# Kernel tuning notes

Measured on AMD Instinct MI355X. Metric: run time of the kernel, lower is better.

Reference implementation:

```python
import jax, jax.numpy as jnp
import numpy as np

DIM = 512
HEADS = 8
DH = DIM // HEADS          # 64
M = DIM // 2               # 256 landmarks
PINV_ITERS = 6
KERNEL = 33                # residual_conv_kernel (lucidrains default)
SCALE = DH ** -0.5
LN_EPS = 1e-5


def setup_inputs() -> dict:
    key = jax.random.key(0)
    ks = jax.random.split(key, 6)
    b, n = 4, 4096
    x = jax.random.normal(ks[0], (b, n, DIM), jnp.float32)
    ln_w = jnp.ones((DIM,), jnp.float32)
    ln_b = jnp.zeros((DIM,), jnp.float32)
    w_qkv = jax.random.normal(ks[1], (DIM, 3 * DIM), jnp.float32) / np.float32(np.sqrt(DIM))
    w_out = jax.random.normal(ks[2], (DIM, DIM), jnp.float32) / np.float32(np.sqrt(DIM))
    b_out = jnp.zeros((DIM,), jnp.float32)
    # depthwise Conv2d(heads, heads, (33,1), groups=heads, bias=False): OIHW = (8,1,33,1)
    conv_w = jax.random.normal(ks[3], (HEADS, 1, KERNEL, 1), jnp.float32) / np.float32(np.sqrt(KERNEL))
    # admin_torch.as_module(8): residual x*omega + f(x), omega learnable scalar init sqrt(8)
    omega = jnp.asarray(np.sqrt(8.0), jnp.float32)
    return dict(x=x, ln_w=ln_w, ln_b=ln_b, w_qkv=w_qkv, w_out=w_out,
                b_out=b_out, conv_w=conv_w, omega=omega)


def _layernorm(x, w, b):
    mu = x.mean(-1, keepdims=True)
    var = x.var(-1, keepdims=True)
    return (x - mu) * jax.lax.rsqrt(var + LN_EPS) * w + b


def _moore_penrose_pinv(x, iters):
    # Newton-Schulz iteration, exactly as lucidrains nystrom-attention
    abs_x = jnp.abs(x)
    col = abs_x.sum(-1)
    row = abs_x.sum(-2)
    z = jnp.swapaxes(x, -1, -2) / (jnp.max(col) * jnp.max(row))
    I = jnp.eye(x.shape[-1], dtype=x.dtype)
    for _ in range(iters):
        xz = x @ z
        z = 0.25 * z @ (13. * I - xz @ (15. * I - xz @ (7. * I - xz)))
    return z


def reference(x, ln_w, ln_b, w_qkv, w_out, b_out, conv_w, omega):
    b, n, _ = x.shape
    nx = _layernorm(x, ln_w, ln_b)
    qkv = nx @ w_qkv                                # [b, n, 3*dim]
    q, k, v = jnp.split(qkv, 3, axis=-1)
    to_heads = lambda t: t.reshape(b, n, HEADS, DH).transpose(0, 2, 1, 3)  # bhnd
    q = to_heads(q) * SCALE
    k = to_heads(k)
    v = to_heads(v)
    l = n // M                                      # tokens per landmark group
    q_l = q.reshape(b, HEADS, M, l, DH).mean(3)     # [b,h,m,d]
    k_l = k.reshape(b, HEADS, M, l, DH).mean(3)
    sim1 = jnp.einsum('bhid,bhjd->bhij', q, k_l)    # [b,h,n,m]
    sim2 = jnp.einsum('bhid,bhjd->bhij', q_l, k_l)  # [b,h,m,m]
    sim3 = jnp.einsum('bhid,bhjd->bhij', q_l, k)    # [b,h,m,n]
    a1 = jax.nn.softmax(sim1, -1)
    a2 = jax.nn.softmax(sim2, -1)
    a3 = jax.nn.softmax(sim3, -1)
    a2_inv = _moore_penrose_pinv(a2, PINV_ITERS)
    out = (a1 @ a2_inv) @ (a3 @ v)                  # [b,h,n,d]
    # residual depthwise conv along the sequence dim of v
    res = jax.lax.conv_general_dilated(
        v, conv_w, window_strides=(1, 1),
        padding=((KERNEL // 2, KERNEL // 2), (0, 0)),
        dimension_numbers=('NCHW', 'OIHW', 'NCHW'),
        feature_group_count=HEADS)
    out = out + res
    out = out.transpose(0, 2, 1, 3).reshape(b, n, HEADS * DH)
    out = out @ w_out + b_out                       # to_out (dropout is eval no-op)
    return x * omega + out                          # admin residual
```

## Files before the change

kernel.cpp:

```cpp
#include <hip/hip_runtime.h>
#include <math.h>

#define B_    4
#define N_    4096
#define DIM_  512
#define H_    8
#define DH_   64
#define M_    256
#define LGRP  16
#define BH_   (B_*H_)
#define SCALE_ 0.125f
#define LN_EPS_ 1e-5f

#define SZ_QKVH (B_*H_*N_*DH_)
#define SZ_LM   (BH_*M_*DH_)
#define SZ_MM   (BH_*M_*M_)

typedef unsigned short ushort_t;
typedef __attribute__((ext_vector_type(8))) short bfrag8;
typedef __attribute__((ext_vector_type(4))) float fvec4;

__device__ __forceinline__ ushort_t f2b(float f) {
    unsigned u = __float_as_uint(f);
    unsigned r = (u + 0x7fffu + ((u >> 16) & 1u)) >> 16;
    return (ushort_t)r;
}
__device__ __forceinline__ float b2f(ushort_t s) {
    return __uint_as_float(((unsigned)s) << 16);
}

__device__ __forceinline__ void gload16(const ushort_t* g, ushort_t* l) {
    __builtin_amdgcn_global_load_lds(
        (const __attribute__((address_space(1))) void*)g,
        (__attribute__((address_space(3))) void*)l, 16, 0, 0);
}

__global__ __launch_bounds__(256) void ln_kernel(const float* __restrict__ x,
                                                 const float* __restrict__ w,
                                                 const float* __restrict__ bb,
                                                 ushort_t* __restrict__ nxb) {
    int row = blockIdx.x;
    int t = threadIdx.x;
    const float* xr = x + (size_t)row * DIM_;
    float v0 = xr[t], v1 = xr[t + 256];
    float s = v0 + v1, sq = v0 * v0 + v1 * v1;
    __shared__ float ls[4], lq[4];
    for (int off = 32; off > 0; off >>= 1) {
        s  += __shfl_down(s, off);
        sq += __shfl_down(sq, off);
    }
    int wid = t >> 6, lid = t & 63;
    if (lid == 0) { ls[wid] = s; lq[wid] = sq; }
    __syncthreads();
    if (t == 0) {
        float S = 0, Q = 0;
        for (int i = 0; i < 4; i++) { S += ls[i]; Q += lq[i]; }
        ls[0] = S; lq[0] = Q;
    }
    __syncthreads();
    float mean = ls[0] * (1.f / DIM_);
    float var  = lq[0] * (1.f / DIM_) - mean * mean;
    float rs = rsqrtf(var + LN_EPS_);
    ushort_t* o = nxb + (size_t)row * DIM_;
    o[t]       = f2b((v0 - mean) * rs * w[t]       + bb[t]);
    o[t + 256] = f2b((v1 - mean) * rs * w[t + 256] + bb[t + 256]);
}

__global__ __launch_bounds__(256) void tcast(const float* __restrict__ in,
                                             ushort_t* __restrict__ outT,
                                             int R, int C) {
    __shared__ float tile[32][33];
    int c0 = blockIdx.x * 32, r0 = blockIdx.y * 32;
    int t = threadIdx.x;
    #pragma unroll
    for (int u = 0; u < 4; u++) {
        int lin = t + 256 * u;
        int r = lin >> 5, c = lin & 31;
        tile[r][c] = in[(size_t)(r0 + r) * C + c0 + c];
    }
    __syncthreads();
    #pragma unroll
    for (int u = 0; u < 4; u++) {
        int lin = t + 256 * u;
        int cc = lin >> 5, rr = lin & 31;
        outT[(size_t)(c0 + cc) * R + r0 + rr] = f2b(tile[rr][cc]);
    }
}

template<int EPI>
__global__ __launch_bounds__(256) void gemm_bt128(const ushort_t* __restrict__ A,
                                                  const ushort_t* __restrict__ BT,
                                                  ushort_t* __restrict__ qb,
                                                  ushort_t* __restrict__ kb,
                                                  ushort_t* __restrict__ vb,
                                                  const float* __restrict__ x,
                                                  const float* __restrict__ bo,
                                                  const float* __restrict__ omega,
                                                  float* __restrict__ out) {
    const int K = 512;
    __shared__ __align__(16) ushort_t smem[4 * 128 * 64];
    int t = threadIdx.x;
    int lin = blockIdx.x + blockIdx.y * gridDim.x;
    int nwg = gridDim.x * gridDim.y;
    int wg  = (lin & 7) * (nwg >> 3) + (lin >> 3);
    int n0 = (wg % gridDim.x) * 128, m0 = (wg / gridDim.x) * 128;
    int w = t >> 6, lane = t & 63;
    int wr = (w >> 1) * 64, wc = (w & 1) * 64;
    int l15 = lane & 15, quad = lane >> 4, kq = quad * 8;
    int lrow = lane >> 3, lc8 = (lane & 7) * 8;
    int scol = lc8 ^ ((lrow & 7) << 3);
    int sw   = (l15 & 7) << 3;
    fvec4 acc[4][4] = {};

    auto stage = [&](int buf, int kc) {
        ushort_t* Ad = smem + buf * 16384;
        ushort_t* Bd = Ad + 8192;
        #pragma unroll
        for (int u = 0; u < 4; u++) {
            int r0 = (w << 5) + (u << 3);
            int row = r0 + lrow;
            const ushort_t* ga;
            if (EPI == 0) {
                ga = A + (size_t)(m0 + row) * K + kc + scol;
            } else {
                int grow = m0 + row; int b_ = grow >> 12, nn = grow & 4095;
                ga = A + (((size_t)(b_ * H_ + (kc >> 6)) * N_ + nn) << 6) + scol;
            }
            gload16(ga, Ad + r0 * 64);
            gload16(BT + (size_t)(n0 + row) * K + kc + scol, Bd + r0 * 64);
        }
    };

    stage(0, 0);
    __syncthreads();
    int cur = 0;
    for (int kt = 0; kt < 8; ++kt) {
        if (kt < 7) stage(cur ^ 1, (kt + 1) * 64);
        const ushort_t* As = smem + cur * 16384;
        const ushort_t* Bs = As + 8192;
        #pragma unroll
        for (int ks = 0; ks < 64; ks += 32) {
            int kcol = (ks + kq) ^ sw;
            bfrag8 a[4], b[4];
            #pragma unroll
            for (int r = 0; r < 4; r++) a[r] = *(bfrag8*)(As + (wr + r * 16 + l15) * 64 + kcol);
            #pragma unroll
            for (int c = 0; c < 4; c++) b[c] = *(bfrag8*)(Bs + (wc + c * 16 + l15) * 64 + kcol);
            #pragma unroll
            for (int r = 0; r < 4; r++)
                #pragma unroll
                for (int c = 0; c < 4; c++)
                    acc[r][c] = __builtin_amdgcn_mfma_f32_16x16x32_bf16(a[r], b[c], acc[r][c], 0, 0, 0);
        }
        __syncthreads();
        cur ^= 1;
    }

    if (EPI == 0) {
        int sec = n0 >> 9;
        float mul = (sec == 0) ? SCALE_ : 1.0f;
        ushort_t (*Ct)[132] = (ushort_t(*)[132])smem;
        #pragma unroll
        for (int r = 0; r < 4; r++) {
            #pragma unroll
            for (int reg = 0; reg < 4; reg++) {
                int lr = wr + r * 16 + quad * 4 + reg;
                #pragma unroll
                for (int c = 0; c < 4; c++) {
                    int lc = wc + c * 16 + l15;
                    Ct[lr][lc] = f2b(acc[r][c][reg] * mul);
                }
            }
        }
        __syncthreads();
        int row = t & 127, half = t >> 7;
        int grow = m0 + row; int b_ = grow >> 12, nn = grow & 4095;
        int head = ((n0 & 511) >> 6) + half;
        ushort_t* dstbuf = (sec == 0) ? qb : ((sec == 1) ? kb : vb);
        ushort_t* dp = dstbuf + (((size_t)(b_ * H_ + head) * N_ + nn) << 6);
        #pragma unroll
        for (int i = 0; i < 8; i++)
            *(uint4*)(dp + i * 8) = *(uint4*)&Ct[row][half * 64 + i * 8];
    } else {
        float om = omega[0];
        #pragma unroll
        for (int r = 0; r < 4; r++) {
            #pragma unroll
            for (int reg = 0; reg < 4; reg++) {
                int grow = m0 + wr + r * 16 + quad * 4 + reg;
                #pragma unroll
                for (int c = 0; c < 4; c++) {
                    int gcol = n0 + wc + c * 16 + l15;
                    size_t o = (size_t)grow * DIM_ + gcol;
                    out[o] = om * x[o] + bo[gcol] + acc[r][c][reg];
                }
            }
        }
    }
}

__global__ __launch_bounds__(256) void landmark_kernel(const ushort_t* __restrict__ q,
                                                       const ushort_t* __restrict__ k,
                                                       ushort_t* __restrict__ ql,
                                                       ushort_t* __restrict__ kl) {
    int idx = blockIdx.x * 256 + threadIdx.x;
    const ushort_t* src = blockIdx.y ? k : q;
    ushort_t* dst = blockIdx.y ? kl : ql;
    int d8 = (idx & 7) * 8;
    int m = (idx >> 3) & 255;
    int bh = idx >> 11;
    const ushort_t* p = src + (((size_t)bh * N_) + m * LGRP) * DH_ + d8;
    float s[8] = {};
    #pragma unroll
    for (int j = 0; j < LGRP; j++) {
        union { uint4 u4; ushort_t sv[8]; } val;
        val.u4 = *(const uint4*)(p + (size_t)j * DH_);
        #pragma unroll
        for (int e = 0; e < 8; e++) s[e] += b2f(val.sv[e]);
    }
    union { uint4 u4; ushort_t sv[8]; } o;
    #pragma unroll
    for (int e = 0; e < 8; e++) o.sv[e] = f2b(s[e] * (1.f / LGRP));
    *(uint4*)(dst + ((size_t)bh * M_ + m) * DH_ + d8) = o.u4;
}

__global__ __launch_bounds__(256) void sim2_softmax(const ushort_t* __restrict__ ql,
                                                    const ushort_t* __restrict__ kl,
                                                    float* __restrict__ a2,
                                                    ushort_t* __restrict__ a2b) {
    int i = blockIdx.x, bh = blockIdx.y, j = threadIdx.x;
    __shared__ float qrow[64];
    __shared__ float red[256];
    if (j < 64) qrow[j] = b2f(ql[((size_t)bh * M_ + i) * DH_ + j]);
    __syncthreads();
    const ushort_t* kr = kl + ((size_t)bh * M_ + j) * DH_;
    float s = 0;
    #pragma unroll
    for (int d = 0; d < 64; d++) s += qrow[d] * b2f(kr[d]);
    red[j] = s; __syncthreads();
    for (int off = 128; off > 0; off >>= 1) {
        if (j < off) red[j] = fmaxf(red[j], red[j + off]);
        __syncthreads();
    }
    float mx = red[0]; __syncthreads();
    float p = __expf(s - mx);
    red[j] = p; __syncthreads();
    for (int off = 128; off > 0; off >>= 1) {
        if (j < off) red[j] += red[j + off];
        __syncthreads();
    }
    float res = p / red[0];
    size_t o = ((size_t)bh * M_ + i) * M_ + j;
    a2[o] = res;
    a2b[o] = f2b(res);
}

__global__ __launch_bounds__(256) void colpart(const float* __restrict__ a2,
                                               float* __restrict__ cs2,
                                               unsigned* __restrict__ red) {
    int bh = blockIdx.x, s = blockIdx.y, t = threadIdx.x;
    if (bh == 0 && s == 0 && t == 0) red[0] = 0u;
    const float* A = a2 + ((size_t)bh << 16) + (size_t)s * 32 * M_;
    float cs = 0.f;
    #pragma unroll
    for (int i = 0; i < 32; i++) cs += A[(size_t)i * M_ + t];
    cs2[((size_t)s * BH_ + bh) * M_ + t] = cs;
}

__global__ __launch_bounds__(256) void colmax(const float* __restrict__ cs2, unsigned* red) {
    int bh = blockIdx.x, t = threadIdx.x;
    float v = 0.f;
    #pragma unroll
    for (int s = 0; s < 8; s++) v += cs2[((size_t)s * BH_ + bh) * M_ + t];
    __shared__ float lr[256];
    lr[t] = v; __syncthreads();
    for (int off = 128; off > 0; off >>= 1) {
        if (t < off) lr[t] = fmaxf(lr[t], lr[t + off]);
        __syncthreads();
    }
    if (t == 0) atomicMax(red, __float_as_uint(lr[0]));
}

__global__ __launch_bounds__(256) void pinv_init2(const float* __restrict__ a2,
                                                  const unsigned* __restrict__ red,
                                                  ushort_t* __restrict__ zA,
                                                  ushort_t* __restrict__ zAT) {
    __shared__ float tile[32][33];
    int bt = blockIdx.z; int j0 = blockIdx.x * 32, i0 = blockIdx.y * 32;
    float invd = 1.f / __uint_as_float(red[0]);
    const float* Ab = a2 + ((size_t)bt << 16);
    size_t bo = (size_t)bt << 16;
    int t = threadIdx.x;
    #pragma unroll
    for (int u = 0; u < 4; u++) {
        int lin = t + 256 * u; int r = lin >> 5, c = lin & 31;
        float vv = Ab[(size_t)(i0 + r) * M_ + j0 + c] * invd;
        tile[r][c] = vv;
        zAT[bo + (size_t)(i0 + r) * M_ + j0 + c] = f2b(vv);
    }
    __syncthreads();
    #pragma unroll
    for (int u = 0; u < 4; u++) {
        int lin = t + 256 * u; int cc = lin >> 5, rr = lin & 31;
        zA[bo + (size_t)(j0 + cc) * M_ + i0 + rr] = f2b(tile[rr][cc]);
    }
}

__global__ __launch_bounds__(256) void gemm_pinv(const ushort_t* __restrict__ A,
                                                 const ushort_t* __restrict__ BT,
                                                 ushort_t* __restrict__ outN,
                                                 ushort_t* __restrict__ outT,
                                                 ushort_t* __restrict__ outT1,
                                                 float* __restrict__ outF,
                                                 float coefI, float scale) {
    __shared__ __align__(16) ushort_t smem[2 * 16384];
    int t = threadIdx.x;
    int lin = blockIdx.x + (blockIdx.y << 2) + (blockIdx.z << 4);
    int wg  = (lin & 7) * 64 + (lin >> 3);
    int n0 = (wg & 3) * 64, m0 = ((wg >> 2) & 3) * 64;
    int bt = wg >> 4;
    const ushort_t* Ab = A + ((size_t)bt << 16);
    const ushort_t* Bb = BT + ((size_t)bt << 16);
    int w = t >> 6, lane = t & 63;
    int wr = (w >> 1) * 32, wc = (w & 1) * 32;
    int l15 = lane & 15, quad = lane >> 4, kq = quad * 8;
    int lrow = lane >> 3, lc8 = (lane & 7) * 8;
    int scol = lc8 ^ ((lrow & 7) << 3);
    int sw   = (l15 & 7) << 3;
    fvec4 acc[2][2] = {};

    #pragma unroll
    for (int c = 0; c < 4; c++) {
        #pragma unroll
        for (int u = 0; u < 2; u++) {
            int r0 = (w << 4) + (u << 3);
            int row = r0 + lrow;
            gload16(Ab + (size_t)(m0 + row) * M_ + c * 64 + scol, smem + c * 4096 + r0 * 64);
            gload16(Bb + (size_t)(n0 + row) * M_ + c * 64 + scol, smem + 16384 + c * 4096 + r0 * 64);
        }
    }
    __syncthreads();

    #pragma unroll
    for (int ks = 0; ks < 256; ks += 32) {
        const ushort_t* As = smem + (ks >> 6) * 4096;
        const ushort_t* Bs = As + 16384;
        int kcol = ((ks & 63) + kq) ^ sw;
        bfrag8 a[2], b[2];
        #pragma unroll
        for (int r = 0; r < 2; r++) a[r] = *(bfrag8*)(As + (wr + r * 16 + l15) * 64 + kcol);
        #pragma unroll
        for (int c = 0; c < 2; c++) b[c] = *(bfrag8*)(Bs + (wc + c * 16 + l15) * 64 + kcol);
        #pragma unroll
        for (int r = 0; r < 2; r++)
            #pragma unroll
            for (int c = 0; c < 2; c++)
                acc[r][c] = __builtin_amdgcn_mfma_f32_16x16x32_bf16(a[r], b[c], acc[r][c], 0, 0, 0);
    }
    __syncthreads();

    size_t bto = (size_t)bt << 16;
    if (outN || outF) {
        #pragma unroll
        for (int r = 0; r < 2; r++) {
            #pragma unroll
            for (int reg = 0; reg < 4; reg++) {
                int grow = m0 + wr + r * 16 + quad * 4 + reg;
                #pragma unroll
                for (int c = 0; c < 2; c++) {
                    int gcol = n0 + wc + c * 16 + l15;
                    float cv = scale * acc[r][c][reg] + (grow == gcol ? coefI : 0.f);
                    if (outN) outN[bto + (size_t)grow * M_ + gcol] = f2b(cv);
                    if (outF) outF[bto + (size_t)grow * M_ + gcol] = cv;
                }
            }
        }
    }
    if (outT || outT1) {
        ushort_t (*Ct)[65] = (ushort_t(*)[65])&smem[0];
        #pragma unroll
        for (int r = 0; r < 2; r++) {
            #pragma unroll
            for (int reg = 0; reg < 4; reg++) {
                int lr = wr + r * 16 + quad * 4 + reg;
                #pragma unroll
                for (int c = 0; c < 2; c++) {
                    int lc = wc + c * 16 + l15;
                    float cv = scale * acc[r][c][reg] + ((m0 + lr) == (n0 + lc) ? coefI : 0.f);
                    Ct[lr][lc] = f2b(cv);
                }
            }
        }
        __syncthreads();
        int j = t & 63, quarter = t >> 6, i0 = quarter * 16;
        #pragma unroll
        for (int vq = 0; vq < 2; vq++) {
            union { uint4 u4; ushort_t s[8]; } o1, o2;
            #pragma unroll
            for (int e = 0; e < 8; e++) {
                int il = i0 + vq * 8 + e;
                ushort_t bv = Ct[il][j];
                o1.s[e] = bv;
                o2.s[e] = f2b(((m0 + il) == (n0 + j) ? 7.f : 0.f) - b2f(bv));
            }
            size_t dst = bto + (size_t)(n0 + j) * M_ + m0 + i0 + vq * 8;
            if (outT)  *(uint4*)&outT[dst]  = o1.u4;
            if (outT1) *(uint4*)&outT1[dst] = o2.u4;
        }
    }
}

__global__ __launch_bounds__(256) void flash_a3v(const ushort_t* __restrict__ Q,
                                                 const ushort_t* __restrict__ K,
                                                 const ushort_t* __restrict__ V,
                                                 float* __restrict__ Opart,
                                                 float* __restrict__ lout) {
    const int nk = N_;
    const int CHUNK = N_ / 8;
    int bh = blockIdx.y, ch = blockIdx.x;
    int j0 = ch * CHUNK, j1 = j0 + CHUNK;

    __shared__ __align__(16) ushort_t smem[4 * 64 * 72];
    ushort_t (*ks)[72]  = (ushort_t(*)[72])smem;
    ushort_t (*vts)[72] = (ushort_t(*)[72])(smem + 64 * 72);
    ushort_t (*pb)[64][72] = (ushort_t(*)[64][72])(smem + 2 * 64 * 72);

    int t = threadIdx.x;
    int w = t >> 6, lane = t & 63;
    int l15 = lane & 15, quad = lane >> 4, kq = quad * 8;
    int wrow = w * 16;

    bfrag8 aq[4][2];
    const ushort_t* Qb = Q + (size_t)bh * M_ * DH_;
    #pragma unroll
    for (int s = 0; s < 4; s++) {
        #pragma unroll
        for (int u = 0; u < 2; u++) {
            int lin = t + 256 * u;
            int r = lin >> 3, cc = (lin & 7) * 8;
            *(uint4*)&pb[0][r][cc] = *(const uint4*)(Qb + (size_t)(s * 64 + r) * DH_ + cc);
        }
        __syncthreads();
        aq[s][0] = *(bfrag8*)&pb[0][wrow + l15][kq];
        aq[s][1] = *(bfrag8*)&pb[0][wrow + l15][32 + kq];
        __syncthreads();
    }

    fvec4 Oacc[4][4];
    #pragma unroll
    for (int s = 0; s < 4; s++)
        #pragma unroll
        for (int nt = 0; nt < 4; nt++)
            #pragma unroll
            for (int reg = 0; reg < 4; reg++) Oacc[s][nt][reg] = 0.f;
    float l_[4][4];
    #pragma unroll
    for (int s = 0; s < 4; s++)
        #pragma unroll
        for (int reg = 0; reg < 4; reg++) l_[s][reg] = 0.f;

    uint4 kreg[2], vreg[2];
    auto loadkv = [&](int j) {
        const ushort_t* Kb = K + ((size_t)bh * nk + j) * DH_;
        const ushort_t* Vb = V + ((size_t)bh * nk + j) * DH_;
        #pragma unroll
        for (int u = 0; u < 2; u++) {
            int lin = t + 256 * u;
            int r = lin >> 3, cc = (lin & 7) * 8;
            kreg[u] = *(const uint4*)(Kb + (size_t)r * DH_ + cc);
            vreg[u] = *(const uint4*)(Vb + (size_t)r * DH_ + cc);
        }
    };

    loadkv(j0);
    for (int j = j0; j < j1; j += 64) {
        #pragma unroll
        for (int u = 0; u < 2; u++) {
            int lin = t + 256 * u;
            int r = lin >> 3, cc = (lin & 7) * 8;
            *(uint4*)&ks[r][cc] = kreg[u];
            union { uint4 u4; ushort_t s[8]; } vv;
            vv.u4 = vreg[u];
            #pragma unroll
            for (int m = 0; m < 8; m++) vts[cc + m][r] = vv.s[m];
        }
        __syncthreads();
        if (j + 64 < j1) loadkv(j + 64);

        bfrag8 kb0[4], kb1[4], vb0[4], vb1[4];
        #pragma unroll
        for (int ct = 0; ct < 4; ct++) {
            kb0[ct] = *(bfrag8*)&ks[ct * 16 + l15][kq];
            kb1[ct] = *(bfrag8*)&ks[ct * 16 + l15][32 + kq];
            vb0[ct] = *(bfrag8*)&vts[ct * 16 + l15][kq];
            vb1[ct] = *(bfrag8*)&vts[ct * 16 + l15][32 + kq];
        }

        #pragma unroll
        for (int s = 0; s < 4; s++) {
            fvec4 S[4];
            #pragma unroll
            for (int ct = 0; ct < 4; ct++)
                #pragma unroll
                for (int reg = 0; reg < 4; reg++) S[ct][reg] = 0.f;
            #pragma unroll
            for (int ct = 0; ct < 4; ct++) {
                S[ct] = __builtin_amdgcn_mfma_f32_16x16x32_bf16(aq[s][0], kb0[ct], S[ct], 0, 0, 0);
                S[ct] = __builtin_amdgcn_mfma_f32_16x16x32_bf16(aq[s][1], kb1[ct], S[ct], 0, 0, 0);
            }
            float ps[4] = {0.f, 0.f, 0.f, 0.f};
            #pragma unroll
            for (int ct = 0; ct < 4; ct++) {
                #pragma unroll
                for (int reg = 0; reg < 4; reg++) {
                    float pv = __expf(S[ct][reg]);
                    ps[reg] += pv;
                    pb[s & 1][wrow + quad * 4 + reg][ct * 16 + l15] = f2b(pv);
                }
            }
            #pragma unroll
            for (int reg = 0; reg < 4; reg++) {
                float sm = ps[reg];
                sm += __shfl_xor(sm, 1);
                sm += __shfl_xor(sm, 2);
                sm += __shfl_xor(sm, 4);
                sm += __shfl_xor(sm, 8);
                l_[s][reg] += sm;
            }
            bfrag8 ap0 = *(bfrag8*)&pb[s & 1][wrow + l15][kq];
            bfrag8 ap1 = *(bfrag8*)&pb[s & 1][wrow + l15][32 + kq];
            #pragma unroll
            for (int nt = 0; nt < 4; nt++) {
                Oacc[s][nt] = __builtin_amdgcn_mfma_f32_16x16x32_bf16(ap0, vb0[nt], Oacc[s][nt], 0, 0, 0);
                Oacc[s][nt] = __builtin_amdgcn_mfma_f32_16x16x32_bf16(ap1, vb1[nt], Oacc[s][nt], 0, 0, 0);
            }
        }
        __syncthreads();
    }

    float (*Of)[68] = (float(*)[68])smem;
    const size_t R = (size_t)BH_ * M_;
    size_t rowbase = (size_t)ch * R + (size_t)bh * M_;
    #pragma unroll
    for (int s = 0; s < 4; s++) {
        __syncthreads();
        #pragma unroll
        for (int reg = 0; reg < 4; reg++) {
            #pragma unroll
            for (int nt = 0; nt < 4; nt++)
                Of[wrow + quad * 4 + reg][nt * 16 + l15] = Oacc[s][nt][reg];
        }
        if (l15 == 0) {
            #pragma unroll
            for (int reg = 0; reg < 4; reg++)
                lout[rowbase + s * 64 + wrow + quad * 4 + reg] = l_[s][reg];
        }
        __syncthreads();
        int orow = t >> 2, oc = (t & 3) * 16;
        float* Od = Opart + (rowbase + s * 64 + orow) * DH_ + oc;
        #pragma unroll
        for (int i = 0; i < 4; i++) {
            float4 v4 = make_float4(Of[orow][oc + i * 4], Of[orow][oc + i * 4 + 1],
                                    Of[orow][oc + i * 4 + 2], Of[orow][oc + i * 4 + 3]);
            *(float4*)(Od + i * 4) = v4;
        }
    }
}

__global__ __launch_bounds__(256) void flash_combine(const float* __restrict__ apart,
                                                     const float* __restrict__ lpart,
                                                     ushort_t* __restrict__ a3vb) {
    int idx = blockIdx.x * 256 + threadIdx.x;
    int d = idx & 63; int row = idx >> 6;
    const int R = BH_ * M_;
    size_t e = (size_t)row * DH_ + d;
    const size_t CH = (size_t)R * DH_;
    float l = 0.f, o = 0.f;
    #pragma unroll
    for (int s = 0; s < 8; s++) {
        l += lpart[row + (size_t)s * R];
        o += apart[e + (size_t)s * CH];
    }
    a3vb[e] = f2b(o / l);
}

__global__ __launch_bounds__(256) void flash_big(const ushort_t* __restrict__ Q,
                                                 const ushort_t* __restrict__ K,
                                                 const ushort_t* __restrict__ VT,
                                                 ushort_t* __restrict__ Obf) {
    const int nq = N_, nk = M_;
    int bh = blockIdx.y;
    int q0 = blockIdx.x * 256;
    __shared__ __align__(16) ushort_t ks[64][72];
    __shared__ __align__(16) ushort_t vts[64][72];
    __shared__ __align__(16) ushort_t pb[2][64][72];

    int t = threadIdx.x;
    int w = t >> 6, lane = t & 63;
    int l15 = lane & 15, quad = lane >> 4, kq = quad * 8;
    int wrow = w * 16;

    bfrag8 aq[4][2];
    const ushort_t* Qb = Q + ((size_t)bh * nq + q0) * DH_;
    #pragma unroll
    for (int s = 0; s < 4; s++) {
        #pragma unroll
        for (int u = 0; u < 2; u++) {
            int lin = t + 256 * u;
            int r = lin >> 3, cc = (lin & 7) * 8;
            *(uint4*)&pb[0][r][cc] = *(const uint4*)(Qb + (size_t)(s * 64 + r) * DH_ + cc);
        }
        __syncthreads();
        aq[s][0] = *(bfrag8*)&pb[0][wrow + l15][kq];
        aq[s][1] = *(bfrag8*)&pb[0][wrow + l15][32 + kq];
        __syncthreads();
    }

    fvec4 Oacc[4][4];
    #pragma unroll
    for (int s = 0; s < 4; s++)
        #pragma unroll
        for (int nt = 0; nt < 4; nt++)
            #pragma unroll
            for (int reg = 0; reg < 4; reg++) Oacc[s][nt][reg] = 0.f;
    float l_[4][4];
    #pragma unroll
    for (int s = 0; s < 4; s++)
        #pragma unroll
        for (int reg = 0; reg < 4; reg++) l_[s][reg] = 0.f;

    const ushort_t* VTb = VT + (size_t)bh * DH_ * nk;
    uint4 kreg[2], vreg[2];
    auto loadkv = [&](int j) {
        const ushort_t* Kb = K + ((size_t)bh * nk + j) * DH_;
        #pragma unroll
        for (int u = 0; u < 2; u++) {
            int lin = t + 256 * u;
            int r = lin >> 3, cc = (lin & 7) * 8;
            kreg[u] = *(const uint4*)(Kb + (size_t)r * DH_ + cc);
            vreg[u] = *(const uint4*)(VTb + (size_t)r * nk + j + cc);
        }
    };

    loadkv(0);
    for (int j = 0; j < nk; j += 64) {
        #pragma unroll
        for (int u = 0; u < 2; u++) {
            int lin = t + 256 * u;
            int r = lin >> 3, cc = (lin & 7) * 8;
            *(uint4*)&ks[r][cc] = kreg[u];
            *(uint4*)&vts[r][cc] = vreg[u];
        }
        __syncthreads();
        if (j + 64 < nk) loadkv(j + 64);

        bfrag8 kb0[4], kb1[4], vb0[4], vb1[4];
        #pragma unroll
        for (int ct = 0; ct < 4; ct++) {
            kb0[ct] = *(bfrag8*)&ks[ct * 16 + l15][kq];
            kb1[ct] = *(bfrag8*)&ks[ct * 16 + l15][32 + kq];
            vb0[ct] = *(bfrag8*)&vts[ct * 16 + l15][kq];
            vb1[ct] = *(bfrag8*)&vts[ct * 16 + l15][32 + kq];
        }

        #pragma unroll
        for (int s = 0; s < 4; s++) {
            fvec4 S[4];
            #pragma unroll
            for (int ct = 0; ct < 4; ct++)
                #pragma unroll
                for (int reg = 0; reg < 4; reg++) S[ct][reg] = 0.f;
            #pragma unroll
            for (int ct = 0; ct < 4; ct++) {
                S[ct] = __builtin_amdgcn_mfma_f32_16x16x32_bf16(aq[s][0], kb0[ct], S[ct], 0, 0, 0);
                S[ct] = __builtin_amdgcn_mfma_f32_16x16x32_bf16(aq[s][1], kb1[ct], S[ct], 0, 0, 0);
            }
            float ps[4] = {0.f, 0.f, 0.f, 0.f};
            #pragma unroll
            for (int ct = 0; ct < 4; ct++) {
                #pragma unroll
                for (int reg = 0; reg < 4; reg++) {
                    float pv = __expf(S[ct][reg]);
                    ps[reg] += pv;
                    pb[s & 1][wrow + quad * 4 + reg][ct * 16 + l15] = f2b(pv);
                }
            }
            #pragma unroll
            for (int reg = 0; reg < 4; reg++) {
                float sm = ps[reg];
                sm += __shfl_xor(sm, 1);
                sm += __shfl_xor(sm, 2);
                sm += __shfl_xor(sm, 4);
                sm += __shfl_xor(sm, 8);
                l_[s][reg] += sm;
            }
            bfrag8 ap0 = *(bfrag8*)&pb[s & 1][wrow + l15][kq];
            bfrag8 ap1 = *(bfrag8*)&pb[s & 1][wrow + l15][32 + kq];
            #pragma unroll
            for (int nt = 0; nt < 4; nt++) {
                Oacc[s][nt] = __builtin_amdgcn_mfma_f32_16x16x32_bf16(ap0, vb0[nt], Oacc[s][nt], 0, 0, 0);
                Oacc[s][nt] = __builtin_amdgcn_mfma_f32_16x16x32_bf16(ap1, vb1[nt], Oacc[s][nt], 0, 0, 0);
            }
        }
        __syncthreads();
    }

    ushort_t* Ob = Obf + ((size_t)bh * nq + q0) * DH_;
    #pragma unroll
    for (int s = 0; s < 4; s++) {
        #pragma unroll
        for (int reg = 0; reg < 4; reg++) {
            float inv = 1.f / l_[s][reg];
            #pragma unroll
            for (int nt = 0; nt < 4; nt++)
                pb[0][wrow + quad * 4 + reg][nt * 16 + l15] = f2b(Oacc[s][nt][reg] * inv);
        }
        __syncthreads();
        #pragma unroll
        for (int u = 0; u < 2; u++) {
            int lin = t + 256 * u;
            int r = lin >> 3, i = (lin & 7) * 8;
            *(uint4*)(Ob + (size_t)(s * 64 + r) * DH_ + i) = *(uint4*)&pb[0][r][i];
        }
        __syncthreads();
    }
}

__global__ __launch_bounds__(256) void wm_mfma(const ushort_t* __restrict__ Z,
                                               const ushort_t* __restrict__ A3V,
                                               ushort_t* __restrict__ WmT) {
    __shared__ __align__(16) ushort_t As[64][72];
    __shared__ __align__(16) ushort_t Bs[64][72];
    int bh = blockIdx.y;
    int i0 = blockIdx.x * 64;
    const ushort_t* Zb = Z + ((size_t)bh << 16);
    const ushort_t* Ab = A3V + ((size_t)bh << 14);
    int t = threadIdx.x;
    int w = t >> 6, lane = t & 63;
    int wr = (w >> 1) * 32, wc = (w & 1) * 32;
    int l15 = lane & 15, quad = lane >> 4, kq = quad * 8;
    fvec4 acc[2][2] = {};
    int rbase = t >> 3, c8 = (t & 7) * 8;

    for (int kc = 0; kc < M_; kc += 64) {
        #pragma unroll
        for (int u = 0; u < 2; u++) {
            int rr = rbase + 32 * u;
            *(float4*)&Bs[rr][c8] = *(const float4*)(Zb + (size_t)(i0 + rr) * M_ + kc + c8);
            union { uint4 u4; ushort_t s[8]; } av;
            av.u4 = *(const uint4*)(Ab + (size_t)(kc + rr) * DH_ + c8);
            #pragma unroll
            for (int m = 0; m < 8; m++) As[c8 + m][rr] = av.s[m];
        }
        __syncthreads();
        #pragma unroll
        for (int ks = 0; ks < 64; ks += 32) {
            bfrag8 a[2], b[2];
            #pragma unroll
            for (int r = 0; r < 2; r++) a[r] = *(bfrag8*)&As[wr + r * 16 + l15][ks + kq];
            #pragma unroll
            for (int c = 0; c < 2; c++) b[c] = *(bfrag8*)&Bs[wc + c * 16 + l15][ks + kq];
            #pragma unroll
            for (int r = 0; r < 2; r++)
                #pragma unroll
                for (int c = 0; c < 2; c++)
                    acc[r][c] = __builtin_amdgcn_mfma_f32_16x16x32_bf16(a[r], b[c], acc[r][c], 0, 0, 0);
        }
        __syncthreads();
    }
    #pragma unroll
    for (int r = 0; r < 2; r++) {
        #pragma unroll
        for (int reg = 0; reg < 4; reg++) {
            int drow = wr + r * 16 + quad * 4 + reg;
            ushort_t* dp = WmT + ((size_t)bh * DH_ + drow) * M_;
            #pragma unroll
            for (int c = 0; c < 2; c++)
                dp[i0 + wc + c * 16 + l15] = f2b(acc[r][c][reg]);
        }
    }
}

__global__ __launch_bounds__(256) void conv_kernel(const ushort_t* __restrict__ V,
                                                   const float* __restrict__ cw,
                                                   const ushort_t* __restrict__ ctxb,
                                                   ushort_t* __restrict__ outb) {
    int bh = blockIdx.y;
    int h = bh & 7;
    int i0 = blockIdx.x * 64;
    __shared__ float vb[96][64];
    __shared__ float wloc[33];
    int t = threadIdx.x;
    if (t < 33) wloc[t] = cw[h * 33 + t];
    #pragma unroll
    for (int u = 0; u < 3; u++) {
        int lin = t + 256 * u;
        int r = lin >> 3, cc = (lin & 7) * 8;
        int gi = i0 - 16 + r;
        union { uint4 u4; ushort_t s[8]; } val;
        if (gi >= 0 && gi < N_)
            val.u4 = *(const uint4*)(V + ((size_t)bh * N_ + gi) * DH_ + cc);
        else
            val.u4 = make_uint4(0, 0, 0, 0);
        #pragma unroll
        for (int m = 0; m < 8; m++) vb[r][cc + m] = b2f(val.s[m]);
    }
    __syncthreads();
    int d = t & 63, rb = t >> 6;
    for (int u = 0; u < 16; u++) {
        int r = rb * 16 + u;
        float s = 0.f;
        #pragma unroll
        for (int kk = 0; kk < 33; kk++) s += wloc[kk] * vb[r + kk][d];
        size_t o = ((size_t)bh * N_ + i0 + r) * DH_ + d;
        outb[o] = f2b(b2f(ctxb[o]) + s);
    }
}

extern "C" void kernel_launch(void* const* d_in, const int* in_sizes, int n_in,
                              void* d_out, int out_size, void* d_ws, size_t ws_size,
                              hipStream_t stream) {
    const float* x      = (const float*)d_in[0];
    const float* ln_w   = (const float*)d_in[1];
    const float* ln_b   = (const float*)d_in[2];
    const float* w_qkv  = (const float*)d_in[3];
    const float* w_out  = (const float*)d_in[4];
    const float* b_out  = (const float*)d_in[5];
    const float* conv_w = (const float*)d_in[6];
    const float* omega  = (const float*)d_in[7];
    float* out = (float*)d_out;

    float* fp = (float*)d_ws;
    float* a2    = fp;              fp += SZ_MM;
    float* apart = fp;              fp += SZ_QKVH / 2;
    float* lpart = fp;              fp += 8 * BH_ * M_;
    float* cs2   = fp;              fp += 8 * BH_ * M_;
    ushort_t* us = (ushort_t*)fp;
    ushort_t* wqkvT = us;           us += DIM_ * 3 * DIM_;
    ushort_t* woT   = us;           us += DIM_ * DIM_;
    ushort_t* a2b   = us;           us += SZ_MM;
    ushort_t* zA    = us;           us += SZ_MM;
    ushort_t* zAT   = us;           us += SZ_MM;
    ushort_t* zB    = us;           us += SZ_MM;
    ushort_t* zBT   = us;           us += SZ_MM;
    ushort_t* qb    = us;           us += SZ_QKVH;
    ushort_t* kb    = us;           us += SZ_QKVH;
    ushort_t* vb    = us;           us += SZ_QKVH;
    ushort_t* ctxb  = us;           us += SZ_QKVH;
    ushort_t* outhb = us;           us += SZ_QKVH;
    ushort_t* ql    = us;           us += SZ_LM;
    ushort_t* kl    = us;           us += SZ_LM;
    ushort_t* WmT   = us;           us += SZ_LM;
    ushort_t* a3vb  = us;           us += SZ_LM;
    unsigned* red   = (unsigned*)us;
    ushort_t* nxb = outhb;
    ushort_t* xz  = ctxb;
    ushort_t* t1T = xz  + SZ_MM;
    ushort_t* t2T = t1T + SZ_MM;
    ushort_t* t3T = t2T + SZ_MM;

    ln_kernel<<<B_ * N_, 256, 0, stream>>>(x, ln_w, ln_b, nxb);
    tcast<<<dim3(48, 16), 256, 0, stream>>>(w_qkv, wqkvT, DIM_, 3 * DIM_);
    tcast<<<dim3(16, 16), 256, 0, stream>>>(w_out, woT, DIM_, DIM_);
    gemm_bt128<0><<<dim3(12, 128), 256, 0, stream>>>(nxb, wqkvT, qb, kb, vb,
                                                     nullptr, nullptr, nullptr, nullptr);
    landmark_kernel<<<dim3(256, 2), 256, 0, stream>>>(qb, kb, ql, kl);
    sim2_softmax<<<dim3(M_, BH_), 256, 0, stream>>>(ql, kl, a2, a2b);
    colpart<<<dim3(BH_, 8), 256, 0, stream>>>(a2, cs2, red);
    colmax<<<BH_, 256, 0, stream>>>(cs2, red);
    pinv_init2<<<dim3(8, 8, 32), 256, 0, stream>>>(a2, red, zA, zAT);

    ushort_t* za = zA;  ushort_t* zaT = zAT;
    ushort_t* zb = zB;  ushort_t* zbT = zBT;
    for (int it = 0; it < 6; it++) {
        gemm_pinv<<<dim3(4, 4, BH_), 256, 0, stream>>>(a2b, zaT, xz, nullptr, t1T, nullptr, 0.f, 1.f);
        gemm_pinv<<<dim3(4, 4, BH_), 256, 0, stream>>>(xz, t1T, nullptr, t2T, nullptr, nullptr, 15.f, -1.f);
        gemm_pinv<<<dim3(4, 4, BH_), 256, 0, stream>>>(xz, t2T, nullptr, t3T, nullptr, nullptr, 13.f, -1.f);
        gemm_pinv<<<dim3(4, 4, BH_), 256, 0, stream>>>(za, t3T, zb, (it < 5) ? zbT : nullptr,
                                                       nullptr, nullptr, 0.f, 0.25f);
        ushort_t* tp;
        tp = za; za = zb; zb = tp;
        tp = zaT; zaT = zbT; zbT = tp;
    }

    flash_a3v<<<dim3(8, BH_), 256, 0, stream>>>(ql, kb, vb, apart, lpart);
    flash_combine<<<(BH_ * M_ * DH_) / 256, 256, 0, stream>>>(apart, lpart, a3vb);
    wm_mfma<<<dim3(4, BH_), 256, 0, stream>>>(za, a3vb, WmT);
    flash_big<<<dim3(N_ / 256, BH_), 256, 0, stream>>>(qb, kl, WmT, ctxb);
    conv_kernel<<<dim3(N_ / 64, BH_), 256, 0, stream>>>(vb, conv_w, ctxb, outhb);
    gemm_bt128<1><<<dim3(4, 128), 256, 0, stream>>>(outhb, woT, nullptr, nullptr, nullptr,
                                                    x, b_out, omega, out);
}
```

Baseline: 471.7 us.

## Fuse depthwise residual conv into flash_big epilogue and drop conv kernel

The 33-tap depthwise convolution over V is now computed in flash_big's output epilogue. Each block stages a 96-row bf16 V window in shared memory, writes the normalized attention output as fp32 to shared memory, and adds the conv sum before storing bf16 once. This removes the separate conv kernel launch and the bf16 round-trip of the intermediate context tensor through global memory. It also drops one bf16 rounding of the context before the add. The risk is that the V staging buffer is aliased onto ks but is larger than ks, so it relies on the following shared arrays lying contiguously. The epilogue also runs a serial 33-tap loop per 64-row slice inside the attention kernel.

```diff
diff --git a/kernel.cpp b/kernel.cpp
--- a/kernel.cpp
+++ b/kernel.cpp
@@ -587,6 +587,8 @@
 __global__ __launch_bounds__(256) void flash_big(const ushort_t* __restrict__ Q,
                                                  const ushort_t* __restrict__ K,
                                                  const ushort_t* __restrict__ VT,
+                                                 const ushort_t* __restrict__ V,
+                                                 const float* __restrict__ cw,
                                                  ushort_t* __restrict__ Obf) {
     const int nq = N_, nk = M_;
     int bh = blockIdx.y;
@@ -594,11 +596,13 @@
     __shared__ __align__(16) ushort_t ks[64][72];
     __shared__ __align__(16) ushort_t vts[64][72];
     __shared__ __align__(16) ushort_t pb[2][64][72];
+    __shared__ float wloc[33];
 
     int t = threadIdx.x;
     int w = t >> 6, lane = t & 63;
     int l15 = lane & 15, quad = lane >> 4, kq = quad * 8;
     int wrow = w * 16;
+    if (t < 33) wloc[t] = cw[(bh & 7) * 33 + t];
 
     bfrag8 aq[4][2];
     const ushort_t* Qb = Q + ((size_t)bh * nq + q0) * DH_;
@@ -705,24 +709,42 @@
         __syncthreads();
     }
 
+    ushort_t (*vstg)[64] = (ushort_t(*)[64])&ks[0][0];
+    float (*Of)[68] = (float(*)[68])&pb[0][0][0];
     ushort_t* Ob = Obf + ((size_t)bh * nq + q0) * DH_;
+    const ushort_t* Vb = V + (size_t)bh * nq * DH_;
+    int d = t & 63, rb = t >> 6;
     #pragma unroll
     for (int s = 0; s < 4; s++) {
+        __syncthreads();
+        #pragma unroll
+        for (int u = 0; u < 3; u++) {
+            int lin = t + 256 * u;
+            int r = lin >> 3, cc = (lin & 7) * 8;
+            int gi = q0 + 64 * s - 16 + r;
+            union { uint4 u4; ushort_t sv[8]; } val;
+            if (gi >= 0 && gi < N_)
+                val.u4 = *(const uint4*)(Vb + (size_t)gi * DH_ + cc);
+            else
+                val.u4 = make_uint4(0, 0, 0, 0);
+            *(uint4*)&vstg[r][cc] = val.u4;
+        }
         #pragma unroll
         for (int reg = 0; reg < 4; reg++) {
             float inv = 1.f / l_[s][reg];
             #pragma unroll
             for (int nt = 0; nt < 4; nt++)
-                pb[0][wrow + quad * 4 + reg][nt * 16 + l15] = f2b(Oacc[s][nt][reg] * inv);
-        }
-        __syncthreads();
-        #pragma unroll
-        for (int u = 0; u < 2; u++) {
-            int lin = t + 256 * u;
-            int r = lin >> 3, i = (lin & 7) * 8;
-            *(uint4*)(Ob + (size_t)(s * 64 + r) * DH_ + i) = *(uint4*)&pb[0][r][i];
-        }
-        __syncthreads();
+                Of[wrow + quad * 4 + reg][nt * 16 + l15] = Oacc[s][nt][reg] * inv;
+        }
+        __syncthreads();
+        #pragma unroll
+        for (int u = 0; u < 16; u++) {
+            int r = rb * 16 + u;
+            float cs = 0.f;
+            #pragma unroll
+            for (int kk = 0; kk < 33; kk++) cs += wloc[kk] * b2f(vstg[r + kk][d]);
+            Ob[(size_t)(s * 64 + r) * DH_ + d] = f2b(Of[r][d] + cs);
+        }
     }
 }
 
@@ -778,42 +800,6 @@
             for (int c = 0; c < 2; c++)
                 dp[i0 + wc + c * 16 + l15] = f2b(acc[r][c][reg]);
         }
-    }
-}
-
-__global__ __launch_bounds__(256) void conv_kernel(const ushort_t* __restrict__ V,
-                                                   const float* __restrict__ cw,
-                                                   const ushort_t* __restrict__ ctxb,
-                                                   ushort_t* __restrict__ outb) {
-    int bh = blockIdx.y;
-    int h = bh & 7;
-    int i0 = blockIdx.x * 64;
-    __shared__ float vb[96][64];
-    __shared__ float wloc[33];
-    int t = threadIdx.x;
-    if (t < 33) wloc[t] = cw[h * 33 + t];
-    #pragma unroll
-    for (int u = 0; u < 3; u++) {
-        int lin = t + 256 * u;
-        int r = lin >> 3, cc = (lin & 7) * 8;
-        int gi = i0 - 16 + r;
-        union { uint4 u4; ushort_t s[8]; } val;
-        if (gi >= 0 && gi < N_)
-            val.u4 = *(const uint4*)(V + ((size_t)bh * N_ + gi) * DH_ + cc);
-        else
-            val.u4 = make_uint4(0, 0, 0, 0);
-        #pragma unroll
-        for (int m = 0; m < 8; m++) vb[r][cc + m] = b2f(val.s[m]);
-    }
-    __syncthreads();
-    int d = t & 63, rb = t >> 6;
-    for (int u = 0; u < 16; u++) {
-        int r = rb * 16 + u;
-        float s = 0.f;
-        #pragma unroll
-        for (int kk = 0; kk < 33; kk++) s += wloc[kk] * vb[r + kk][d];
-        size_t o = ((size_t)bh * N_ + i0 + r) * DH_ + d;
-        outb[o] = f2b(b2f(ctxb[o]) + s);
     }
 }
 
@@ -885,9 +871,8 @@
 
     flash_a3v<<<dim3(8, BH_), 256, 0, stream>>>(ql, kb, vb, apart, lpart);
     flash_combine<<<(BH_ * M_ * DH_) / 256, 256, 0, stream>>>(apart, lpart, a3vb);
-    wm_mfma<<<dim3(4, BH_), 256, 0, stream>>>(za, a3vb, WmT);
-    flash_big<<<dim3(N_ / 256, BH_), 256, 0, stream>>>(qb, kl, WmT, ctxb);
-    conv_kernel<<<dim3(N_ / 64, BH_), 256, 0, stream>>>(vb, conv_w, ctxb, outhb);
+    wm_mfma<<<dim3(4, BH_), 256, 0, stream>>>(zA, a3vb, WmT);
+    flash_big<<<dim3(N_ / 256, BH_), 256, 0, stream>>>(qb, kl, WmT, vb, conv_w, outhb);
     gemm_bt128<1><<<dim3(4, 128), 256, 0, stream>>>(outhb, woT, nullptr, nullptr, nullptr,
                                                     x, b_out, omega, out);
 }
```

New measurement: 548.2 us. 1.16x slower.
